# Kernel tuning notes

Measured on AMD Instinct MI355X. Metric: run time of the kernel, lower is better.

## Reference

```python
import jax, jax.numpy as jnp
import numpy as np

B, IC, OC, K, H, W = 8, 512, 512, 3, 32, 32
GAIN, LRMUL = 1.0, 1.0
# compute_runtime_coef: fan_in = prod(weight_shape[:-1])
RC_CONV = GAIN / np.sqrt(K * K * IC) * LRMUL   # conv weight [K,K,IC,OC]
RC_DENSE = GAIN / np.sqrt(IC) * LRMUL          # dense weight [IC, IC]


def setup_inputs() -> dict:
    key = jax.random.key(0)
    ks = jax.random.split(key, 4)
    x = jax.random.normal(ks[0], (B, IC, H, W), dtype=jnp.float32)
    w = jax.random.normal(ks[1], (B, IC), dtype=jnp.float32)
    # init_std = 1/lrmul = 1.0 for both weights; bias init zeros
    conv_w = jax.random.normal(ks[2], (K, K, IC, OC), dtype=jnp.float32)
    dense_w = jax.random.normal(ks[3], (IC, IC), dtype=jnp.float32)
    dense_b = jnp.zeros((IC,), dtype=jnp.float32)
    return {"x": x, "w": w, "conv_w": conv_w, "dense_w": dense_w, "dense_b": dense_b}


def reference(x, w, conv_w, dense_w, dense_b):
    b, ic, h, wd = x.shape
    # modulation: style = Dense(w) + bias + 1
    style = w @ (RC_DENSE * dense_w) + LRMUL * dense_b + 1.0        # [B, IC]
    wt = (RC_CONV * conv_w)[None] * style[:, None, None, :, None]   # [B,K,K,IC,OC]
    # demodulation: rsqrt of sum of squares over (kh, kw, ic)
    d = jax.lax.rsqrt(jnp.sum(jnp.square(wt), axis=(1, 2, 3)) + 1e-8)  # [B, OC]
    wt = wt * d[:, None, None, None, :]
    # grouped conv with groups = batch: weight -> OIHW [B*OC, IC, K, K]
    w_g = jnp.transpose(wt, (0, 4, 3, 1, 2)).reshape(b * OC, ic, K, K)
    xg = x.reshape(1, b * ic, h, wd)
    y = jax.lax.conv_general_dilated(
        xg, w_g, window_strides=(1, 1), padding="SAME",
        dimension_numbers=("NCHW", "OIHW", "NCHW"), feature_group_count=b)
    return y.reshape(b, OC, h, wd)
```

## Files before the change

kernel.cpp:

```cpp
#include <hip/hip_runtime.h>
#include <stdint.h>


#define B_   8
#define IC_  512
#define OC_  512

static constexpr float RC_DENSE = 0.04419417382415922f;
static constexpr float RC_CONV  = 0.014731391274719739f;

typedef _Float16 half8    __attribute__((ext_vector_type(8)));
typedef float    floatx16 __attribute__((ext_vector_type(16)));

__device__ __forceinline__ void g2l(const void* g, void* l) {
  __builtin_amdgcn_global_load_lds(
      (const __attribute__((address_space(1))) void*)g,
      (__attribute__((address_space(3))) void*)l, 16, 0, 0);
}

__global__ __launch_bounds__(256) void style_kernel(
    const float* __restrict__ wv, const float* __restrict__ dw,
    const float* __restrict__ db, float* __restrict__ sm,
    float* __restrict__ sm2) {
  const int b = blockIdx.y;
  const int i = blockIdx.x * 64 + (threadIdx.x & 63);
  const int jg = threadIdx.x >> 6;
  __shared__ float red[4][64];
  float p = 0.f;
  for (int j = jg * 128; j < jg * 128 + 128; ++j)
    p += wv[b * IC_ + j] * dw[(size_t)j * IC_ + i];
  red[jg][threadIdx.x & 63] = p;
  __syncthreads();
  if (threadIdx.x < 64) {
    float s = red[0][threadIdx.x] + red[1][threadIdx.x] +
              red[2][threadIdx.x] + red[3][threadIdx.x];
    s = s * RC_DENSE + db[i] + 1.0f;
    float v = s * RC_CONV;
    sm[b * IC_ + i] = v;
    sm2[b * IC_ + i] = v * v;
  }
}

__global__ __launch_bounds__(256) void prep_kernel(
    const float* __restrict__ cw, const float* __restrict__ x,
    const float* __restrict__ sm, const float* __restrict__ sm2,
    _Float16* __restrict__ Wtf, float* __restrict__ dpart,
    _Float16* __restrict__ xsp) {
  __shared__ __align__(16) char smem[33280];
  const int bid = blockIdx.x;
  const int tid = threadIdx.x;
  if (bid < 256) {
    _Float16* LA = (_Float16*)smem;
    float* redall = (float*)(smem + 18432);
    const int by2 = bid >> 4, icb = bid & 15;
    const int by = by2 >> 1, h2 = by2 & 1;
    const int oc0 = by * 64 + h2 * 32, ic0 = icb * 32;
    const int ocl = tid & 31, g = tid >> 5;
    float sq4[4] = {};
    for (int m = 0; m < 36; ++m) {
      int r = m * 8 + g;
      int t = r >> 5, icl = r & 31;
      float v = cw[(size_t)(t * IC_ + ic0 + icl) * OC_ + oc0 + ocl];
      sq4[m & 3] += v * v;
      LA[m * 256 + ocl * 8 + g] = (_Float16)v;
    }
    for (int b = 0; b < 8; ++b) {
      float p = 0.f;
      for (int s = 0; s < 4; ++s)
        p += sm2[b * IC_ + ic0 + g + 8 * s] * sq4[s];
      redall[(b * 8 + g) * 32 + ocl] = p;
    }
    __syncthreads();
    _Float16* dst = Wtf + (size_t)(by * 16 + icb) * 18432;
    for (int it = 0; it < 5; ++it) {
      int c = it * 256 + tid;
      if (c < 1152) {
        int m = c >> 5, o2 = c & 31;
        *(half8*)(dst + (size_t)(m * 64 + h2 * 32 + o2) * 8) =
            *(const half8*)&LA[m * 256 + o2 * 8];
      }
    }
    const int bb = tid >> 5, o3 = tid & 31;
    float s = 0.f;
    for (int g2 = 0; g2 < 8; ++g2) s += redall[(bb * 8 + g2) * 32 + o3];
    dpart[(size_t)icb * 4096 + bb * OC_ + oc0 + o3] = s;
  } else {
    _Float16* Xt = (_Float16*)smem;
    const int rb = bid - 256;
    const int b = rb >> 5, h = rb & 31;
    for (int k = 0; k < 16; ++k) {
      int idx = k * 256 + tid;
      int ic = idx >> 3, wc = (idx & 7) * 4;
      float4 v = *(const float4*)&x[((size_t)(b * IC_ + ic) * 32 + h) * 32 + wc];
      float s = sm[b * IC_ + ic];
      Xt[(wc + 0) * 520 + ic] = (_Float16)(v.x * s);
      Xt[(wc + 1) * 520 + ic] = (_Float16)(v.y * s);
      Xt[(wc + 2) * 520 + ic] = (_Float16)(v.z * s);
      Xt[(wc + 3) * 520 + ic] = (_Float16)(v.w * s);
    }
    __syncthreads();
    _Float16* xb = xsp + (size_t)b * 16 * 36992;
    const int r = h + 1;
    half8 z = {};
    for (int it = 0; it < 9; ++it) {
      int c = it * 256 + tid;
      if (c < 2176) {
        int icb = c / 136, rem = c - 136 * icb, kkq = rem / 34, C = rem - 34 * kkq;
        half8 val = z;
        if (C != 0 && C != 33)
          val = *(const half8*)&Xt[(C - 1) * 520 + icb * 32 + kkq * 8];
        *(half8*)&xb[(size_t)icb * 36992 + (size_t)r * 1088 + kkq * 272 + C * 8] = val;
      }
    }
    if (h == 0 || h == 31) {
      const int rz = (h == 0) ? 0 : 33;
      for (int it = 0; it < 9; ++it) {
        int c = it * 256 + tid;
        if (c < 2176) {
          int icb = c / 136, rem = c - 136 * icb, kkq = rem / 34, C = rem - 34 * kkq;
          *(half8*)&xb[(size_t)icb * 36992 + (size_t)rz * 1088 + kkq * 272 + C * 8] = z;
        }
      }
    }
  }
}

__global__ __launch_bounds__(256, 4) void conv_kernel(
    const _Float16* __restrict__ Wtf,
    const _Float16* __restrict__ xsp,
    const float* __restrict__ dpart,
    float* __restrict__ out) {
  const int byq = blockIdx.x & 7, hoc = blockIdx.x >> 3;
  const int bx = blockIdx.y, b = blockIdx.z;
  const int tid = threadIdx.x, lane = tid & 63, w = tid >> 6;
  const int n = lane & 31, kq = lane >> 5;
  const int h0 = bx * 4;

  __shared__ __align__(16) _Float16 As[2][4608];
  __shared__ __align__(16) _Float16 Xs[2][3264];
  __shared__ float redd[8][32];
  __shared__ float dvl[32];

  const _Float16* gX = xsp + (size_t)b * 16 * 36992 + (size_t)h0 * 1088;
  const _Float16* gA = Wtf + (size_t)byq * 16 * 18432 + hoc * 256;

  const int nA = (w == 0) ? 3 : 2;
  const int iA = (w == 0) ? 0 : 1 + 2 * w;

  auto stage = [&](int st, int p) {
    const int icb = st >> 1, kk = st & 1;
    const _Float16* a = gA + (size_t)icb * 18432 + kk * 1024;
    for (int k = 0; k < nA; ++k) {
      int c = (iA + k) * 64 + lane;
      int r = c >> 5, o2 = c & 31;
      g2l(a + ((r >> 1) * 4 + (r & 1)) * 512 + o2 * 8, &As[p][c * 8]);
    }
    const _Float16* xg = gX + (size_t)icb * 36992 + kk * 544;
    {
      int c = w * 102 + lane;
      int r = c / 68, o = c - r * 68;
      g2l(xg + r * 1088 + o * 8, &Xs[p][c * 8]);
      c += 64;
      if (lane < 38) {
        int r2 = c / 68, o2x = c - r2 * 68;
        g2l(xg + r2 * 1088 + o2x * 8, &Xs[p][c * 8]);
      }
    }
  };

  floatx16 acc = {};
  stage(0, 0);
  for (int st = 0; st < 32; ++st) {
    const int cur = st & 1;
    __syncthreads();
    if (st + 1 < 32) stage(st + 1, cur ^ 1);
    const _Float16* Ap = &As[cur][0] + kq * 256 + n * 8;
    const _Float16* Xp = &Xs[cur][0] + w * 544 + kq * 272 + n * 8;
    half8 a[9];
#pragma unroll
    for (int t = 0; t < 9; ++t) a[t] = *(const half8*)(Ap + t * 512);
#pragma unroll
    for (int s = 0; s < 3; ++s) {
#pragma unroll
      for (int kw = 0; kw < 3; ++kw) {
        half8 xv = *(const half8*)(Xp + s * 544 + kw * 8);
        acc = __builtin_amdgcn_mfma_f32_32x32x16_f16(a[s * 3 + kw], xv, acc,
                                                     0, 0, 0);
      }
    }
  }

  const int oc0 = byq * 64 + hoc * 32;
  __syncthreads();
  {
    const int oc_l = tid & 31, ig = tid >> 5;
    float s = dpart[(size_t)(ig * 2) * 4096 + b * OC_ + oc0 + oc_l] +
              dpart[(size_t)(ig * 2 + 1) * 4096 + b * OC_ + oc0 + oc_l];
    redd[ig][oc_l] = s;
  }
  __syncthreads();
  if (tid < 32) {
    float s = 1e-8f;
#pragma unroll
    for (int g = 0; g < 8; ++g) s += redd[g][tid];
    dvl[tid] = rsqrtf(s);
  }
  __syncthreads();
#pragma unroll
  for (int rg = 0; rg < 16; ++rg) {
    const int row = (rg & 3) + 8 * (rg >> 2) + 4 * kq;
    float* op = out + ((size_t)b * OC_ + oc0 + row) * 1024 + (h0 + w) * 32 + n;
    op[0] = acc[rg] * dvl[row];
  }
}

extern "C" void kernel_launch(void* const* d_in, const int* in_sizes, int n_in,
                              void* d_out, int out_size, void* d_ws, size_t ws_size,
                              hipStream_t stream) {
  const float* x       = (const float*)d_in[0];
  const float* w       = (const float*)d_in[1];
  const float* conv_w  = (const float*)d_in[2];
  const float* dense_w = (const float*)d_in[3];
  const float* dense_b = (const float*)d_in[4];
  float* out = (float*)d_out;

  char* ws = (char*)d_ws;
  float*    sm    = (float*)ws;
  float*    sm2   = (float*)(ws + (16 << 10));
  float*    dpart = (float*)(ws + (32 << 10));
  _Float16* Wtf   = (_Float16*)(ws + (288 << 10));
  _Float16* xsp   = (_Float16*)(ws + (288 << 10) + 4718592);

  style_kernel<<<dim3(8, B_), 256, 0, stream>>>(w, dense_w, dense_b, sm, sm2);
  prep_kernel<<<512, 256, 0, stream>>>(conv_w, x, sm, sm2, Wtf, dpart, xsp);
  conv_kernel<<<dim3(16, 8, B_), 256, 0, stream>>>(Wtf, xsp, dpart, out);
}
```

Measured before the change: 135.0 us.

## Rebalance async LDS loads across waves and use partial vmcnt waits

Redistributes the global-to-LDS staging so every wave issues exactly four loads per stage: waves 0-1 load weights, wave 2 loads the remaining weights plus some input rows, and wave 3 loads the rest of the input. The __syncthreads at the top of each iteration becomes an explicit s_waitcnt vmcnt(4) plus s_barrier, so the next stage's loads stay in flight while the current buffer is consumed. A second barrier after the MFMAs guards buffer reuse. The change relies on the per-wave load count staying exactly four, and wave 3 issuing a lane-predicated load; if the counts drift the partial waitcnt becomes unsafe.

Measured after the change: 132.9 us. About the same (-1.6%).

```diff
diff --git a/kernel.cpp b/kernel.cpp
--- a/kernel.cpp
+++ b/kernel.cpp
@@ -144,26 +144,42 @@
   const _Float16* gX = xsp + (size_t)b * 16 * 36992 + (size_t)h0 * 1088;
   const _Float16* gA = Wtf + (size_t)byq * 16 * 18432 + hoc * 256;
 
-  const int nA = (w == 0) ? 3 : 2;
-  const int iA = (w == 0) ? 0 : 1 + 2 * w;
-
   auto stage = [&](int st, int p) {
     const int icb = st >> 1, kk = st & 1;
     const _Float16* a = gA + (size_t)icb * 18432 + kk * 1024;
-    for (int k = 0; k < nA; ++k) {
-      int c = (iA + k) * 64 + lane;
-      int r = c >> 5, o2 = c & 31;
-      g2l(a + ((r >> 1) * 4 + (r & 1)) * 512 + o2 * 8, &As[p][c * 8]);
-    }
     const _Float16* xg = gX + (size_t)icb * 36992 + kk * 544;
-    {
-      int c = w * 102 + lane;
-      int r = c / 68, o = c - r * 68;
-      g2l(xg + r * 1088 + o * 8, &Xs[p][c * 8]);
-      c += 64;
-      if (lane < 38) {
-        int r2 = c / 68, o2x = c - r2 * 68;
-        g2l(xg + r2 * 1088 + o2x * 8, &Xs[p][c * 8]);
+    if (w < 2) {
+#pragma unroll
+      for (int k = 0; k < 4; ++k) {
+        int c = (w * 4 + k) * 64 + lane;
+        int r = c >> 5, o2 = c & 31;
+        g2l(a + ((r >> 1) * 4 + (r & 1)) * 512 + o2 * 8, &As[p][c * 8]);
+      }
+    } else if (w == 2) {
+      {
+        int c = 8 * 64 + lane;
+        int r = c >> 5, o2 = c & 31;
+        g2l(a + ((r >> 1) * 4 + (r & 1)) * 512 + o2 * 8, &As[p][c * 8]);
+      }
+#pragma unroll
+      for (int k = 0; k < 3; ++k) {
+        int c = k * 64 + lane;
+        int r = c / 68, o = c - r * 68;
+        g2l(xg + r * 1088 + o * 8, &Xs[p][c * 8]);
+      }
+    } else {
+#pragma unroll
+      for (int k = 0; k < 3; ++k) {
+        int c = (3 + k) * 64 + lane;
+        int r = c / 68, o = c - r * 68;
+        g2l(xg + r * 1088 + o * 8, &Xs[p][c * 8]);
+      }
+      {
+        int c = 6 * 64 + lane;
+        if (lane < 24) {
+          int r = c / 68, o = c - r * 68;
+          g2l(xg + r * 1088 + o * 8, &Xs[p][c * 8]);
+        }
       }
     }
   };
@@ -172,8 +188,14 @@
   stage(0, 0);
   for (int st = 0; st < 32; ++st) {
     const int cur = st & 1;
-    __syncthreads();
-    if (st + 1 < 32) stage(st + 1, cur ^ 1);
+    if (st + 1 < 32) {
+      stage(st + 1, cur ^ 1);
+      asm volatile("s_waitcnt vmcnt(4)" ::: "memory");
+    } else {
+      asm volatile("s_waitcnt vmcnt(0)" ::: "memory");
+    }
+    __builtin_amdgcn_s_barrier();
+    __builtin_amdgcn_sched_barrier(0);
     const _Float16* Ap = &As[cur][0] + kq * 256 + n * 8;
     const _Float16* Xp = &Xs[cur][0] + w * 544 + kq * 272 + n * 8;
     half8 a[9];
@@ -188,6 +210,8 @@
                                                      0, 0, 0);
       }
     }
+    __builtin_amdgcn_sched_barrier(0);
+    __builtin_amdgcn_s_barrier();
   }
 
   const int oc0 = byq * 64 + hoc * 32;
```

## Compute two output rows per wave with register-resident X and explicit waitcnt pipelining

Applied to the files above, without the earlier changes.

Each block now covers 8 output rows instead of 4, and each wave computes two rows with two accumulators. This reuses every weight fragment in LDS across 2 rows and halves the per-output A traffic. The X input no longer goes through LDS: each wave loads its 4 padded rows directly from global memory into registers, double-buffered across stages. Manual vmcnt waits, sched barriers and setprio are added to overlap loads with MFMA. The grid halves and launch bounds drop to 2 waves per SIMD, which raises register pressure and lowers occupancy, and the hardcoded vmcnt counts are fragile.

Result: slower. 139.2 us (+3.1%).

```diff
diff --git a/kernel.cpp b/kernel.cpp
--- a/kernel.cpp
+++ b/kernel.cpp
@@ -125,7 +125,58 @@
   }
 }
 
-__global__ __launch_bounds__(256, 4) void conv_kernel(
+
+#define LOADX(XV, ST)                                                        \
+  {                                                                          \
+    const _Float16* xb_ =                                                    \
+        gXw + (size_t)((ST) >> 1) * 36992 + ((ST) & 1) * 544;                \
+    _Pragma("unroll")                                                        \
+    for (int s_ = 0; s_ < 4; ++s_)                                           \
+      _Pragma("unroll")                                                      \
+      for (int kw_ = 0; kw_ < 3; ++kw_)                                      \
+        XV[s_][kw_] = *(const half8*)(xb_ + s_ * 1088 + kw_ * 8);            \
+  }
+
+#define COMPUTE(XV, CUR)                                                     \
+  {                                                                          \
+    const _Float16* Ap = &As[CUR][0] + kq * 256 + n * 8;                     \
+    half8 a_[9];                                                             \
+    _Pragma("unroll")                                                        \
+    for (int t_ = 0; t_ < 9; ++t_) a_[t_] = *(const half8*)(Ap + t_ * 512);  \
+    __builtin_amdgcn_s_setprio(1);                                           \
+    _Pragma("unroll")                                                        \
+    for (int s_ = 0; s_ < 4; ++s_)                                           \
+      _Pragma("unroll")                                                      \
+      for (int kw_ = 0; kw_ < 3; ++kw_)                                      \
+        _Pragma("unroll")                                                    \
+        for (int kh_ = 0; kh_ < 3; ++kh_) {                                  \
+          int j_ = s_ - kh_;                                                 \
+          if (j_ >= 0 && j_ < 2)                                             \
+            acc[j_] = __builtin_amdgcn_mfma_f32_32x32x16_f16(                \
+                a_[kh_ * 3 + kw_], XV[s_][kw_], acc[j_], 0, 0, 0);           \
+        }                                                                    \
+    __builtin_amdgcn_s_setprio(0);                                           \
+  }
+
+#define STEP(ST, CUR, XVU, XVN)                                              \
+  {                                                                          \
+    if ((ST) + 1 < 32) {                                                     \
+      stageA((ST) + 1, (CUR) ^ 1);          \
+      LOADX(XVN, (ST) + 1)                                                   \
+      __builtin_amdgcn_sched_barrier(0);                                     \
+      asm volatile("s_waitcnt vmcnt(27)" ::: "memory");                      \
+    } else {                                                                 \
+      __builtin_amdgcn_sched_barrier(0);                                     \
+      asm volatile("s_waitcnt vmcnt(12)" ::: "memory");                      \
+    }                                                                        \
+    __builtin_amdgcn_s_barrier();                                            \
+    __builtin_amdgcn_sched_barrier(0);                                       \
+    COMPUTE(XVU, CUR)                                                        \
+    __builtin_amdgcn_sched_barrier(0);                                       \
+    __builtin_amdgcn_s_barrier();                                            \
+  }
+
+__global__ __launch_bounds__(256, 2) void conv_kernel(
     const _Float16* __restrict__ Wtf,
     const _Float16* __restrict__ xsp,
     const float* __restrict__ dpart,
@@ -134,60 +185,36 @@
   const int bx = blockIdx.y, b = blockIdx.z;
   const int tid = threadIdx.x, lane = tid & 63, w = tid >> 6;
   const int n = lane & 31, kq = lane >> 5;
-  const int h0 = bx * 4;
+  const int h0 = bx * 8;
 
   __shared__ __align__(16) _Float16 As[2][4608];
-  __shared__ __align__(16) _Float16 Xs[2][3264];
   __shared__ float redd[8][32];
   __shared__ float dvl[32];
 
-  const _Float16* gX = xsp + (size_t)b * 16 * 36992 + (size_t)h0 * 1088;
   const _Float16* gA = Wtf + (size_t)byq * 16 * 18432 + hoc * 256;
-
-  const int nA = (w == 0) ? 3 : 2;
-  const int iA = (w == 0) ? 0 : 1 + 2 * w;
-
-  auto stage = [&](int st, int p) {
+  const _Float16* gXw = xsp + (size_t)b * 16 * 36992 +
+                        (size_t)(h0 + 2 * w) * 1088 + kq * 272 + n * 8;
+
+  auto stageA = [&](int st, int p) {
     const int icb = st >> 1, kk = st & 1;
     const _Float16* a = gA + (size_t)icb * 18432 + kk * 1024;
-    for (int k = 0; k < nA; ++k) {
-      int c = (iA + k) * 64 + lane;
-      int r = c >> 5, o2 = c & 31;
-      g2l(a + ((r >> 1) * 4 + (r & 1)) * 512 + o2 * 8, &As[p][c * 8]);
-    }
-    const _Float16* xg = gX + (size_t)icb * 36992 + kk * 544;
-    {
-      int c = w * 102 + lane;
-      int r = c / 68, o = c - r * 68;
-      g2l(xg + r * 1088 + o * 8, &Xs[p][c * 8]);
-      c += 64;
-      if (lane < 38) {
-        int r2 = c / 68, o2x = c - r2 * 68;
-        g2l(xg + r2 * 1088 + o2x * 8, &Xs[p][c * 8]);
+    if (lane < 48) {
+#pragma unroll
+      for (int k = 0; k < 3; ++k) {
+        int c = (w * 3 + k) * 48 + lane;
+        int r = c >> 5, o2 = c & 31;
+        g2l(a + ((r >> 1) * 4 + (r & 1)) * 512 + o2 * 8, &As[p][c * 8]);
       }
     }
   };
 
-  floatx16 acc = {};
-  stage(0, 0);
-  for (int st = 0; st < 32; ++st) {
-    const int cur = st & 1;
-    __syncthreads();
-    if (st + 1 < 32) stage(st + 1, cur ^ 1);
-    const _Float16* Ap = &As[cur][0] + kq * 256 + n * 8;
-    const _Float16* Xp = &Xs[cur][0] + w * 544 + kq * 272 + n * 8;
-    half8 a[9];
-#pragma unroll
-    for (int t = 0; t < 9; ++t) a[t] = *(const half8*)(Ap + t * 512);
-#pragma unroll
-    for (int s = 0; s < 3; ++s) {
-#pragma unroll
-      for (int kw = 0; kw < 3; ++kw) {
-        half8 xv = *(const half8*)(Xp + s * 544 + kw * 8);
-        acc = __builtin_amdgcn_mfma_f32_32x32x16_f16(a[s * 3 + kw], xv, acc,
-                                                     0, 0, 0);
-      }
-    }
+  floatx16 acc[2] = {};
+  half8 xvA[4][3], xvB[4][3];
+  stageA(0, 0);
+  LOADX(xvA, 0)
+  for (int ii = 0; ii < 32; ii += 2) {
+    STEP(ii,     0, xvA, xvB)
+    STEP(ii + 1, 1, xvB, xvA)
   }
 
   const int oc0 = byq * 64 + hoc * 32;
@@ -206,11 +233,14 @@
     dvl[tid] = rsqrtf(s);
   }
   __syncthreads();
+  const int r0 = h0 + 2 * w;
 #pragma unroll
   for (int rg = 0; rg < 16; ++rg) {
     const int row = (rg & 3) + 8 * (rg >> 2) + 4 * kq;
-    float* op = out + ((size_t)b * OC_ + oc0 + row) * 1024 + (h0 + w) * 32 + n;
-    op[0] = acc[rg] * dvl[row];
+    const float dv = dvl[row];
+    float* op = out + ((size_t)b * OC_ + oc0 + row) * 1024 + r0 * 32 + n;
+    op[0]  = acc[0][rg] * dv;
+    op[32] = acc[1][rg] * dv;
   }
 }
 
@@ -233,5 +263,5 @@
 
   style_kernel<<<dim3(8, B_), 256, 0, stream>>>(w, dense_w, dense_b, sm, sm2);
   prep_kernel<<<512, 256, 0, stream>>>(conv_w, x, sm, sm2, Wtf, dpart, xsp);
-  conv_kernel<<<dim3(16, 8, B_), 256, 0, stream>>>(Wtf, xsp, dpart, out);
-}
+  conv_kernel<<<dim3(16, 4, B_), 256, 0, stream>>>(Wtf, xsp, dpart, out);
+}
```
